# Kernel optimization log

Hardware: AMD Instinct MI355X
Metric: run time of the kernel (lower is better)

Reference implementation:

```python
import jax, jax.numpy as jnp
import numpy as np

N_NODES = 100000
N_EDGES = 1000000
IN_DIM = 64
OUT_DIM = 64
EDGE_DIM = 16
LN_EPS = 1e-5
GINE_EPS = 0.0  # PyG GINEConv default eps


def setup_inputs() -> dict:
    key = jax.random.key(0)
    ks = jax.random.split(key, 10)
    s = lambda d: 1.0 / np.sqrt(d)
    x = jax.random.normal(ks[0], (N_NODES, IN_DIM), dtype=jnp.float32)
    edge_index = jax.random.randint(ks[1], (2, N_EDGES), 0, N_NODES, dtype=jnp.int64)
    edge_attr = jax.random.normal(ks[2], (N_EDGES, EDGE_DIM), dtype=jnp.float32)
    # GINEConv internal edge projection Linear(edge_dim, in_dim)
    We = jax.random.uniform(ks[3], (EDGE_DIM, IN_DIM), jnp.float32, -s(EDGE_DIM), s(EDGE_DIM))
    be = jax.random.uniform(ks[4], (IN_DIM,), jnp.float32, -s(EDGE_DIM), s(EDGE_DIM))
    # MLP: Linear(in_dim, out_dim) -> ReLU -> Linear(out_dim, out_dim)
    W1 = jax.random.uniform(ks[5], (IN_DIM, OUT_DIM), jnp.float32, -s(IN_DIM), s(IN_DIM))
    b1 = jax.random.uniform(ks[6], (OUT_DIM,), jnp.float32, -s(IN_DIM), s(IN_DIM))
    W2 = jax.random.uniform(ks[7], (OUT_DIM, OUT_DIM), jnp.float32, -s(OUT_DIM), s(OUT_DIM))
    b2 = jax.random.uniform(ks[8], (OUT_DIM,), jnp.float32, -s(OUT_DIM), s(OUT_DIM))
    ln_gamma = jnp.ones((OUT_DIM,), jnp.float32)
    ln_beta = jnp.zeros((OUT_DIM,), jnp.float32)
    return {"x": x, "edge_index": edge_index, "edge_attr": edge_attr,
            "We": We, "be": be, "W1": W1, "b1": b1, "W2": W2, "b2": b2,
            "ln_gamma": ln_gamma, "ln_beta": ln_beta}


def reference(x, edge_index, edge_attr, We, be, W1, b1, W2, b2, ln_gamma, ln_beta):
    src, dst = edge_index[0], edge_index[1]
    # message: ReLU(x_j + lin(edge_attr))  [E, IN_DIM]
    msg = jax.nn.relu(x[src] + edge_attr @ We + be)
    # scatter-sum into target nodes  [N, IN_DIM]
    aggr = jax.ops.segment_sum(msg, dst, num_segments=x.shape[0])
    h = (1.0 + GINE_EPS) * x + aggr
    # MLP
    h = jax.nn.relu(h @ W1 + b1) @ W2 + b2
    # LayerNorm over last dim
    mu = jnp.mean(h, axis=-1, keepdims=True)
    var = jnp.var(h, axis=-1, keepdims=True)
    h = (h - mu) * jax.lax.rsqrt(var + LN_EPS) * ln_gamma + ln_beta
    return jax.nn.relu(h)
```

## Files before the change

### kernel.cpp

```cpp
#include <hip/hip_runtime.h>

typedef short short8 __attribute__((ext_vector_type(8)));
typedef float f32x4 __attribute__((ext_vector_type(4)));

__device__ __forceinline__ float bf2f(unsigned short b) {
    union { unsigned u; float f; } c;
    c.u = ((unsigned)b) << 16;
    return c.f;
}

__device__ __forceinline__ unsigned short f2bf(float x) {
    union { float f; unsigned u; } c;
    c.f = x;
    unsigned u = c.u;
    u += 0x7fffu + ((u >> 16) & 1u);
    return (unsigned short)(u >> 16);
}

__device__ __forceinline__ float loadf(const void* p, long long i, unsigned isbf) {
    if (isbf) return bf2f(((const unsigned short*)p)[i]);
    return ((const float*)p)[i];
}

__device__ __forceinline__ f32x4 mfma16(short8 a, short8 b, f32x4 c) {
    return __builtin_amdgcn_mfma_f32_16x16x32_bf16(a, b, c, 0, 0, 0);
}

__global__ void gine_flag_kernel(const unsigned* gm_bits, const unsigned* ei_bits,
                                 unsigned* flags) {
    if (blockIdx.x == 0 && threadIdx.x == 0) {
        flags[0] = (gm_bits[0] == 0x3F803F80u) ? 1u : 0u;
        unsigned o = 0;
        for (int k = 0; k < 8; ++k) o |= ei_bits[2 * k + 1];
        flags[1] = (o == 0u) ? 1u : 0u;
    }
}

__global__ void gine_zero_kernel(float* aggr, int n) {
    int t = blockIdx.x * blockDim.x + threadIdx.x;
    if (t < n) aggr[t] = 0.0f;
}

__global__ void gine_prep_kernel(const void* W1, const void* b1,
                                 const void* W2, const void* b2,
                                 const void* gm, const void* bt,
                                 const unsigned* flags,
                                 unsigned short* W1B, unsigned short* W2B,
                                 float* vecs) {
    int t = blockIdx.x * blockDim.x + threadIdx.x;
    unsigned isbf = flags[0];
    if (t < 8192) {
        int which = t >> 12;
        int u = t & 4095;
        int j = u & 7, L = (u >> 3) & 63, ktnt = u >> 9;
        int kt = ktnt >> 2, nt = ktnt & 3;
        int k = kt * 32 + (L >> 4) * 8 + j;
        int c = nt * 16 + (L & 15);
        const void* W = which ? W2 : W1;
        unsigned short v = f2bf(loadf(W, k * 64 + c, isbf));
        if (which) W2B[u] = v; else W1B[u] = v;
    } else if (t < 8448) {
        int u = t - 8192;
        const void* s = (u < 64) ? b1 : (u < 128) ? b2 : (u < 192) ? gm : bt;
        vecs[u] = loadf(s, u & 63, isbf);
    }
}

__global__ void GINEBlock_49795850830259_kernel(
    const void* x, const void* edge_index, const void* edge_attr,
    const void* We, const void* be, const unsigned* flags,
    float* aggr, int E, int N, int n0, int n1) {
    int wid  = (blockIdx.x * blockDim.x + threadIdx.x) >> 6;
    int lane = threadIdx.x & 63;
    if (wid >= E) return;

    unsigned isbf = flags[0];
    unsigned is64 = flags[1];

    long long src, dst;
    if (is64) {
        src = ((const long long*)edge_index)[wid];
        dst = ((const long long*)edge_index)[E + wid];
    } else {
        src = ((const int*)edge_index)[wid];
        dst = ((const int*)edge_index)[E + wid];
    }
    if (src < 0 || src >= N || dst < n0 || dst >= n1) return;

    float eav = 0.0f;
    if (lane < 16) eav = loadf(edge_attr, (long long)wid * 16 + lane, isbf);

    float acc = loadf(be, lane, isbf);
    for (int k = 0; k < 16; ++k)
        acc += __shfl(eav, k, 64) * loadf(We, k * 64 + lane, isbf);

    acc += loadf(x, src * 64 + lane, isbf);
    if (acc < 0.0f) acc = 0.0f;

    atomicAdd(aggr + (dst - n0) * 64 + lane, acc);
}

__global__ __launch_bounds__(256) void gine_node_mfma_kernel(
    const void* x, const float* aggr,
    const unsigned short* W1B, const unsigned short* W2B,
    const float* vecs, const unsigned* flags,
    void* out, int n0, int n1) {
    __shared__ float Tlds[4][16 * 68];
    int w = threadIdx.x >> 6;
    int L = threadIdx.x & 63;
    int g = L >> 4, m = L & 15;
    int nb = n0 + (blockIdx.x * 4 + w) * 16;
    if (nb >= n1) return;
    unsigned isbf = flags[0];

    const float* b1f = vecs;
    const float* b2f = vecs + 64;
    const float* gmf = vecs + 128;
    const float* btf = vecs + 192;

    int node = nb + m;
    if (node >= n1) node = n1 - 1;
    long long rel = node - n0;

    short8 ahi[2], alo[2];
    for (int kt = 0; kt < 2; ++kt) {
        int fb = kt * 32 + g * 8;
        const float* ap = aggr + rel * 64 + fb;
        f32x4 a0 = *(const f32x4*)ap;
        f32x4 a1 = *(const f32x4*)(ap + 4);
        float xv[8];
        if (isbf) {
            const unsigned short* xp = (const unsigned short*)x + (long long)node * 64 + fb;
            uint4 xb = *(const uint4*)xp;
            unsigned ww[4] = {xb.x, xb.y, xb.z, xb.w};
            for (int q = 0; q < 4; ++q) {
                xv[2 * q]     = bf2f((unsigned short)(ww[q] & 0xffffu));
                xv[2 * q + 1] = bf2f((unsigned short)(ww[q] >> 16));
            }
        } else {
            const float* xp = (const float*)x + (long long)node * 64 + fb;
            f32x4 x0 = *(const f32x4*)xp;
            f32x4 x1 = *(const f32x4*)(xp + 4);
            for (int j = 0; j < 4; ++j) { xv[j] = x0[j]; xv[4 + j] = x1[j]; }
        }
        for (int j = 0; j < 8; ++j) {
            float aval = (j < 4) ? a0[j] : a1[j - 4];
            float h = xv[j] + aval;
            unsigned short hb = f2bf(h);
            float lo = h - bf2f(hb);
            ahi[kt][j] = (short)hb;
            alo[kt][j] = (short)f2bf(lo);
        }
    }

    float t16[16];
    for (int nt = 0; nt < 4; ++nt) {
        short8 bp0 = *(const short8*)(W1B + ((size_t)(0 * 4 + nt) * 64 + L) * 8);
        short8 bp1 = *(const short8*)(W1B + ((size_t)(1 * 4 + nt) * 64 + L) * 8);
        f32x4 acc = {0.f, 0.f, 0.f, 0.f};
        acc = mfma16(ahi[0], bp0, acc);
        acc = mfma16(ahi[1], bp1, acc);
        acc = mfma16(alo[0], bp0, acc);
        acc = mfma16(alo[1], bp1, acc);
        float bias = b1f[nt * 16 + m];
        for (int r = 0; r < 4; ++r) {
            float v = acc[r] + bias;
            t16[nt * 4 + r] = v > 0.f ? v : 0.f;
        }
    }

    float* tl = Tlds[w];
    for (int nt = 0; nt < 4; ++nt)
        for (int r = 0; r < 4; ++r)
            tl[(g * 4 + r) * 68 + nt * 16 + m] = t16[nt * 4 + r];

    short8 thi[2], tlo[2];
    for (int kt = 0; kt < 2; ++kt) {
        const float* rp = tl + m * 68 + kt * 32 + g * 8;
        f32x4 v0 = *(const f32x4*)rp;
        f32x4 v1 = *(const f32x4*)(rp + 4);
        for (int j = 0; j < 8; ++j) {
            float h = (j < 4) ? v0[j] : v1[j - 4];
            unsigned short hb = f2bf(h);
            float lo = h - bf2f(hb);
            thi[kt][j] = (short)hb;
            tlo[kt][j] = (short)f2bf(lo);
        }
    }

    float o16[16];
    for (int nt = 0; nt < 4; ++nt) {
        short8 bp0 = *(const short8*)(W2B + ((size_t)(0 * 4 + nt) * 64 + L) * 8);
        short8 bp1 = *(const short8*)(W2B + ((size_t)(1 * 4 + nt) * 64 + L) * 8);
        f32x4 acc = {0.f, 0.f, 0.f, 0.f};
        acc = mfma16(thi[0], bp0, acc);
        acc = mfma16(thi[1], bp1, acc);
        acc = mfma16(tlo[0], bp0, acc);
        acc = mfma16(tlo[1], bp1, acc);
        float bias = b2f[nt * 16 + m];
        for (int r = 0; r < 4; ++r) o16[nt * 4 + r] = acc[r] + bias;
    }

    for (int r = 0; r < 4; ++r) {
        float s = o16[r] + o16[4 + r] + o16[8 + r] + o16[12 + r];
        s += __shfl_xor(s, 1, 64);
        s += __shfl_xor(s, 2, 64);
        s += __shfl_xor(s, 4, 64);
        s += __shfl_xor(s, 8, 64);
        float mu = s * (1.0f / 64.0f);
        float v = 0.f;
        for (int nt = 0; nt < 4; ++nt) {
            float d = o16[nt * 4 + r] - mu;
            v += d * d;
        }
        v += __shfl_xor(v, 1, 64);
        v += __shfl_xor(v, 2, 64);
        v += __shfl_xor(v, 4, 64);
        v += __shfl_xor(v, 8, 64);
        float inv = rsqrtf(v * (1.0f / 64.0f) + 1e-5f);
        int nodeR = nb + g * 4 + r;
        if (nodeR < n1) {
            for (int nt = 0; nt < 4; ++nt) {
                int c = nt * 16 + m;
                float rr = (o16[nt * 4 + r] - mu) * inv * gmf[c] + btf[c];
                if (rr < 0.f) rr = 0.f;
                long long oidx = (long long)nodeR * 64 + c;
                if (isbf) ((unsigned short*)out)[oidx] = f2bf(rr);
                else      ((float*)out)[oidx] = rr;
            }
        }
    }
}

extern "C" void kernel_launch(void* const* d_in, const int* in_sizes, int n_in,
                              void* d_out, int out_size, void* d_ws, size_t ws_size,
                              hipStream_t stream) {
    const void* x          = d_in[0];
    const void* edge_index = d_in[1];
    const void* edge_attr  = d_in[2];
    const void* We         = d_in[3];
    const void* be         = d_in[4];
    const void* W1         = d_in[5];
    const void* b1         = d_in[6];
    const void* W2         = d_in[7];
    const void* b2         = d_in[8];
    const void* gm         = d_in[9];
    const void* bt         = d_in[10];

    const int N = in_sizes[0] / 64;
    const int E = in_sizes[1] / 2;

    unsigned* flags     = (unsigned*)d_ws;
    unsigned short* W1B = (unsigned short*)((char*)d_ws + 256);
    unsigned short* W2B = W1B + 4096;
    float* vecs         = (float*)(W2B + 4096);
    float* aggr         = (float*)((char*)d_ws + 32768);

    long long usable = (ws_size > 32768) ? (long long)(ws_size - 32768) : 0;
    long long ncll = (usable / 256) & ~63LL;
    int NC = (ncll > N) ? N : (int)ncll;
    if (NC < 64) return;

    gine_flag_kernel<<<1, 64, 0, stream>>>((const unsigned*)gm,
                                           (const unsigned*)edge_index, flags);
    gine_prep_kernel<<<33, 256, 0, stream>>>(W1, b1, W2, b2, gm, bt, flags,
                                             W1B, W2B, vecs);

    long long edge_threads = (long long)E * 64;
    int edge_blocks = (int)((edge_threads + 255) / 256);

    for (int n0 = 0; n0 < N; n0 += NC) {
        int n1 = n0 + NC; if (n1 > N) n1 = N;
        int chunk = n1 - n0;

        int n_aggr = chunk * 64;
        gine_zero_kernel<<<(n_aggr + 255) / 256, 256, 0, stream>>>(aggr, n_aggr);

        GINEBlock_49795850830259_kernel<<<edge_blocks, 256, 0, stream>>>(
            x, edge_index, edge_attr, We, be, flags, aggr, E, N, n0, n1);

        int node_blocks = (chunk + 63) / 64;
        gine_node_mfma_kernel<<<node_blocks, 256, 0, stream>>>(
            x, aggr, W1B, W2B, vecs, flags, d_out, n0, n1);
    }
}
```

Measured before the change: 540.1 us.

## Replace atomic scatter-add with CSR sort by destination and per-node gather

Builds a CSR of edges grouped by destination node (histogram, single-block scan, atomic scatter of src/edge id pairs). A gather kernel then has each wave sum messages for one node, adding x itself, and writes h without float atomics. The node MLP kernel now reads the precomputed h. This removes the 64M float atomicAdds but adds several passes over edge_index, a serial single-block scan over 100k nodes, and random edge_attr reads. The old chunked path is kept as a fallback when the workspace is too small.

```diff
diff --git a/kernel.cpp b/kernel.cpp
--- a/kernel.cpp
+++ b/kernel.cpp
@@ -36,14 +36,15 @@
     }
 }
 
-__global__ void gine_zero_kernel(float* aggr, int n) {
+__global__ void gine_zero_kernel(float* p, int n) {
     int t = blockIdx.x * blockDim.x + threadIdx.x;
-    if (t < n) aggr[t] = 0.0f;
+    if (t < n) p[t] = 0.0f;
 }
 
 __global__ void gine_prep_kernel(const void* W1, const void* b1,
                                  const void* W2, const void* b2,
                                  const void* gm, const void* bt,
+                                 const void* We, const void* be,
                                  const unsigned* flags,
                                  unsigned short* W1B, unsigned short* W2B,
                                  float* vecs) {
@@ -63,6 +64,128 @@
         int u = t - 8192;
         const void* s = (u < 64) ? b1 : (u < 128) ? b2 : (u < 192) ? gm : bt;
         vecs[u] = loadf(s, u & 63, isbf);
+    } else if (t < 8512) {
+        vecs[256 + (t - 8448)] = loadf(be, t - 8448, isbf);
+    } else if (t < 9536) {
+        int u = t - 8512;
+        vecs[320 + u] = loadf(We, u, isbf);
+    }
+}
+
+__global__ void gine_hist_kernel(const void* edge_index, const unsigned* flags,
+                                 int* count, int E, int N) {
+    int t = blockIdx.x * blockDim.x + threadIdx.x;
+    int stride = gridDim.x * blockDim.x;
+    unsigned is64 = flags[1];
+    for (int e = t; e < E; e += stride) {
+        long long dst = is64 ? ((const long long*)edge_index)[E + e]
+                             : (long long)((const int*)edge_index)[E + e];
+        if (dst >= 0 && dst < N) atomicAdd(&count[(int)dst], 1);
+    }
+}
+
+__global__ void gine_scan_kernel(const int* count, int* row_start, int* cursor,
+                                 int N) {
+    __shared__ int part[256];
+    __shared__ int base[256];
+    int t = threadIdx.x;
+    int span = (N + 255) >> 8;
+    int lo = t * span;
+    int hi = lo + span;
+    if (lo > N) lo = N;
+    if (hi > N) hi = N;
+    int s = 0;
+    for (int i = lo; i < hi; ++i) s += count[i];
+    part[t] = s;
+    __syncthreads();
+    if (t == 0) {
+        int run = 0;
+        for (int i = 0; i < 256; ++i) { base[i] = run; run += part[i]; }
+    }
+    __syncthreads();
+    int run = base[t];
+    for (int i = lo; i < hi; ++i) {
+        row_start[i] = run;
+        cursor[i] = run;
+        run += count[i];
+    }
+    if (lo < N && hi == N) row_start[N] = run;
+}
+
+__global__ void gine_scatter_kernel(const void* edge_index, const unsigned* flags,
+                                    int* cursor, unsigned long long* sorted,
+                                    int E, int N) {
+    int t = blockIdx.x * blockDim.x + threadIdx.x;
+    int stride = gridDim.x * blockDim.x;
+    unsigned is64 = flags[1];
+    for (int e = t; e < E; e += stride) {
+        long long src, dst;
+        if (is64) {
+            src = ((const long long*)edge_index)[e];
+            dst = ((const long long*)edge_index)[E + e];
+        } else {
+            src = ((const int*)edge_index)[e];
+            dst = ((const int*)edge_index)[E + e];
+        }
+        if (dst < 0 || dst >= N) continue;
+        if (src < 0) src = 0;
+        if (src >= N) src = N - 1;
+        int pos = atomicAdd(&cursor[(int)dst], 1);
+        sorted[pos] = ((unsigned long long)(unsigned)e << 32) | (unsigned long long)(unsigned)src;
+    }
+}
+
+__global__ void gine_gather_kernel(const void* x, const void* edge_attr,
+                                   const unsigned long long* sorted,
+                                   const int* row_start, const float* vecs,
+                                   const unsigned* flags, float* h, int N) {
+    int w = threadIdx.x >> 6;
+    int lane = threadIdx.x & 63;
+    int gw = blockIdx.x * 4 + w;
+    int nwaves = gridDim.x * 4;
+    unsigned isbf = flags[0];
+
+    float Wcol[16];
+    for (int k = 0; k < 16; ++k) Wcol[k] = vecs[320 + k * 64 + lane];
+    float bev = vecs[256 + lane];
+
+    for (int v = gw; v < N; v += nwaves) {
+        float hacc = loadf(x, (long long)v * 64 + lane, isbf);
+        int beg = row_start[v];
+        int end = row_start[v + 1];
+        for (int i = beg; i < end; ++i) {
+            unsigned long long p = sorted[i];
+            int src = (int)(p & 0xffffffffULL);
+            int eid = (int)(p >> 32);
+
+            float xv = loadf(x, (long long)src * 64 + lane, isbf);
+
+            float ea[16];
+            if (isbf) {
+                const uint4* eap = (const uint4*)((const unsigned short*)edge_attr
+                                                  + (size_t)eid * 16);
+                uint4 e0 = eap[0];
+                uint4 e1 = eap[1];
+                unsigned wds[8] = {e0.x, e0.y, e0.z, e0.w, e1.x, e1.y, e1.z, e1.w};
+                for (int q = 0; q < 8; ++q) {
+                    union { unsigned u; float f; } clo, chi;
+                    clo.u = wds[q] << 16;
+                    chi.u = wds[q] & 0xffff0000u;
+                    ea[2 * q]     = clo.f;
+                    ea[2 * q + 1] = chi.f;
+                }
+            } else {
+                const float* eap = (const float*)edge_attr + (size_t)eid * 16;
+                for (int q = 0; q < 16; ++q) ea[q] = eap[q];
+            }
+
+            float msg = bev;
+            for (int k = 0; k < 16; ++k) msg += ea[k] * Wcol[k];
+            msg += xv;
+            if (msg < 0.f) msg = 0.f;
+            hacc += msg;
+        }
+        h[(long long)v * 64 + lane] = hacc;
     }
 }
 
@@ -100,11 +223,18 @@
     atomicAdd(aggr + (dst - n0) * 64 + lane, acc);
 }
 
+__global__ void gine_addx_kernel(const void* x, float* aggr,
+                                 const unsigned* flags, int n0, int n1) {
+    int t = blockIdx.x * blockDim.x + threadIdx.x;
+    int total = (n1 - n0) * 64;
+    if (t >= total) return;
+    unsigned isbf = flags[0];
+    aggr[t] += loadf(x, (long long)n0 * 64 + t, isbf);
+}
+
 __global__ __launch_bounds__(256) void gine_node_mfma_kernel(
-    const void* x, const float* aggr,
-    const unsigned short* W1B, const unsigned short* W2B,
-    const float* vecs, const unsigned* flags,
-    void* out, int n0, int n1) {
+    const float* h, const unsigned short* W1B, const unsigned short* W2B,
+    const float* vecs, const unsigned* flags, void* out, int n0, int n1) {
     __shared__ float Tlds[4][16 * 68];
     int w = threadIdx.x >> 6;
     int L = threadIdx.x & 63;
@@ -125,29 +255,13 @@
     short8 ahi[2], alo[2];
     for (int kt = 0; kt < 2; ++kt) {
         int fb = kt * 32 + g * 8;
-        const float* ap = aggr + rel * 64 + fb;
-        f32x4 a0 = *(const f32x4*)ap;
-        f32x4 a1 = *(const f32x4*)(ap + 4);
-        float xv[8];
-        if (isbf) {
-            const unsigned short* xp = (const unsigned short*)x + (long long)node * 64 + fb;
-            uint4 xb = *(const uint4*)xp;
-            unsigned ww[4] = {xb.x, xb.y, xb.z, xb.w};
-            for (int q = 0; q < 4; ++q) {
-                xv[2 * q]     = bf2f((unsigned short)(ww[q] & 0xffffu));
-                xv[2 * q + 1] = bf2f((unsigned short)(ww[q] >> 16));
-            }
-        } else {
-            const float* xp = (const float*)x + (long long)node * 64 + fb;
-            f32x4 x0 = *(const f32x4*)xp;
-            f32x4 x1 = *(const f32x4*)(xp + 4);
-            for (int j = 0; j < 4; ++j) { xv[j] = x0[j]; xv[4 + j] = x1[j]; }
-        }
+        const float* hp = h + rel * 64 + fb;
+        f32x4 a0 = *(const f32x4*)hp;
+        f32x4 a1 = *(const f32x4*)(hp + 4);
         for (int j = 0; j < 8; ++j) {
-            float aval = (j < 4) ? a0[j] : a1[j - 4];
-            float h = xv[j] + aval;
-            unsigned short hb = f2bf(h);
-            float lo = h - bf2f(hb);
+            float hv = (j < 4) ? a0[j] : a1[j - 4];
+            unsigned short hb = f2bf(hv);
+            float lo = hv - bf2f(hb);
             ahi[kt][j] = (short)hb;
             alo[kt][j] = (short)f2bf(lo);
         }
@@ -180,9 +294,9 @@
         f32x4 v0 = *(const f32x4*)rp;
         f32x4 v1 = *(const f32x4*)(rp + 4);
         for (int j = 0; j < 8; ++j) {
-            float h = (j < 4) ? v0[j] : v1[j - 4];
-            unsigned short hb = f2bf(h);
-            float lo = h - bf2f(hb);
+            float hv = (j < 4) ? v0[j] : v1[j - 4];
+            unsigned short hb = f2bf(hv);
+            float lo = hv - bf2f(hb);
             thi[kt][j] = (short)hb;
             tlo[kt][j] = (short)f2bf(lo);
         }
@@ -232,6 +346,8 @@
     }
 }
 
+static inline size_t align256(size_t a) { return (a + 255) & ~(size_t)255; }
+
 extern "C" void kernel_launch(void* const* d_in, const int* in_sizes, int n_in,
                               void* d_out, int out_size, void* d_ws, size_t ws_size,
                               hipStream_t stream) {
@@ -254,33 +370,62 @@
     unsigned short* W1B = (unsigned short*)((char*)d_ws + 256);
     unsigned short* W2B = W1B + 4096;
     float* vecs         = (float*)(W2B + 4096);
-    float* aggr         = (float*)((char*)d_ws + 32768);
-
+
+    gine_flag_kernel<<<1, 64, 0, stream>>>((const unsigned*)gm,
+                                           (const unsigned*)edge_index, flags);
+    gine_prep_kernel<<<38, 256, 0, stream>>>(W1, b1, W2, b2, gm, bt, We, be,
+                                             flags, W1B, W2B, vecs);
+
+    size_t o_count  = 32768;
+    size_t o_row    = o_count + align256((size_t)N * 4);
+    size_t o_cursor = o_row + align256((size_t)(N + 1) * 4);
+    size_t o_sorted = o_cursor + align256((size_t)N * 4);
+    size_t o_h      = o_sorted + align256((size_t)E * 8);
+    size_t need     = o_h + (size_t)N * 256;
+
+    if (ws_size >= need) {
+        int* count    = (int*)((char*)d_ws + o_count);
+        int* row_start= (int*)((char*)d_ws + o_row);
+        int* cursor   = (int*)((char*)d_ws + o_cursor);
+        unsigned long long* sorted = (unsigned long long*)((char*)d_ws + o_sorted);
+        float* h      = (float*)((char*)d_ws + o_h);
+
+        gine_zero_kernel<<<(N + 255) / 256, 256, 0, stream>>>((float*)count, N);
+        gine_hist_kernel<<<1024, 256, 0, stream>>>(edge_index, flags, count, E, N);
+        gine_scan_kernel<<<1, 256, 0, stream>>>(count, row_start, cursor, N);
+        gine_scatter_kernel<<<1024, 256, 0, stream>>>(edge_index, flags, cursor,
+                                                      sorted, E, N);
+        int gblocks = (N + 15) / 16;
+        if (gblocks > 6250) gblocks = 6250;
+        gine_gather_kernel<<<gblocks, 256, 0, stream>>>(x, edge_attr, sorted,
+                                                        row_start, vecs, flags, h, N);
+        int node_blocks = (N + 63) / 64;
+        gine_node_mfma_kernel<<<node_blocks, 256, 0, stream>>>(
+            h, W1B, W2B, vecs, flags, d_out, 0, N);
+        return;
+    }
+
+    float* aggr = (float*)((char*)d_ws + 32768);
     long long usable = (ws_size > 32768) ? (long long)(ws_size - 32768) : 0;
     long long ncll = (usable / 256) & ~63LL;
     int NC = (ncll > N) ? N : (int)ncll;
     if (NC < 64) return;
 
-    gine_flag_kernel<<<1, 64, 0, stream>>>((const unsigned*)gm,
-                                           (const unsigned*)edge_index, flags);
-    gine_prep_kernel<<<33, 256, 0, stream>>>(W1, b1, W2, b2, gm, bt, flags,
-                                             W1B, W2B, vecs);
-
     long long edge_threads = (long long)E * 64;
     int edge_blocks = (int)((edge_threads + 255) / 256);
 
     for (int n0 = 0; n0 < N; n0 += NC) {
         int n1 = n0 + NC; if (n1 > N) n1 = N;
         int chunk = n1 - n0;
-
         int n_aggr = chunk * 64;
+
         gine_zero_kernel<<<(n_aggr + 255) / 256, 256, 0, stream>>>(aggr, n_aggr);
-
         GINEBlock_49795850830259_kernel<<<edge_blocks, 256, 0, stream>>>(
             x, edge_index, edge_attr, We, be, flags, aggr, E, N, n0, n1);
-
+        gine_addx_kernel<<<(n_aggr + 255) / 256, 256, 0, stream>>>(
+            x, aggr, flags, n0, n1);
         int node_blocks = (chunk + 63) / 64;
         gine_node_mfma_kernel<<<node_blocks, 256, 0, stream>>>(
-            x, aggr, W1B, W2B, vecs, flags, d_out, n0, n1);
-    }
-}
+            aggr, W1B, W2B, vecs, flags, d_out, n0, n1);
+    }
+}
```

Measured after the change: 697.4 us. 29.1% more time.
